# Performance work log

Measured on AMD Instinct MI355X. Metric: run time of the kernel, lower is better.

## Reference

```python
import jax, jax.numpy as jnp
import numpy as np

N = 50000   # nodes
E = 600000  # edges
D = 128     # in_channels == heads*hidden_channels
OUT = 64    # out_channels
L = 3       # local_layers
EPS = 1e-5  # BatchNorm eps


def setup_inputs() -> dict:
    key = jax.random.key(0)
    ks = jax.random.split(key, 10)
    s = 0.05
    x = jax.random.normal(ks[0], (N, D), jnp.float32)
    edge_index = jax.random.randint(ks[1], (2, E), 0, N, dtype=jnp.int32)
    Wg = jax.random.normal(ks[2], (L, D, D), jnp.float32) * s  # GCNConv weights
    bg = jnp.zeros((L, D), jnp.float32)                         # GCNConv biases
    Wl = jax.random.normal(ks[3], (L, D, D), jnp.float32) * s  # residual Linear weights
    bl = jax.random.normal(ks[4], (L, D), jnp.float32) * s
    gamma = jnp.ones((L, D), jnp.float32)                       # BN scale
    beta = jnp.zeros((L, D), jnp.float32)                       # BN shift
    Wp = jax.random.normal(ks[5], (D, OUT), jnp.float32) * s   # pred head
    bp = jnp.zeros((OUT,), jnp.float32)
    return {"x": x, "edge_index": edge_index, "Wg": Wg, "bg": bg,
            "Wl": Wl, "bl": bl, "gamma": gamma, "beta": beta,
            "Wp": Wp, "bp": bp}


def reference(x, edge_index, Wg, bg, Wl, bl, gamma, beta, Wp, bp):
    src, dst = edge_index[0], edge_index[1]
    # GCN symmetric normalization with self-loops (PyG gcn_norm):
    # deg computed on target (col) including self-loop.
    deg = jax.ops.segment_sum(jnp.ones((E,), x.dtype), dst, num_segments=N) + 1.0
    dinv = jax.lax.rsqrt(deg)                      # deg^{-1/2}, [N]
    enorm = dinv[src] * dinv[dst]                  # per-edge norm, [E]
    self_norm = (dinv * dinv)[:, None]             # deg^{-1} for self-loop, [N,1]

    h = x
    x_local = jnp.zeros((N, D), x.dtype)
    for i in range(L):
        hg = h @ Wg[i]                             # [N, D] transformed features
        # gather -> weight -> scatter-add (message passing) + self-loop term
        agg = jax.ops.segment_sum(hg[src] * enorm[:, None], dst, num_segments=N)
        conv = agg + hg * self_norm + bg[i]
        # residual linear
        h = conv + h @ Wl[i] + bl[i]
        # BatchNorm1d (training-mode batch statistics, biased var)
        mu = jnp.mean(h, axis=0)
        var = jnp.mean(jnp.square(h - mu), axis=0)
        h = (h - mu) * jax.lax.rsqrt(var + EPS) * gamma[i] + beta[i]
        h = jax.nn.relu(h)
        x_local = x_local + h                      # add_ accumulation
    return x_local @ Wp + bp
```

## Files before the change

kernel.cpp:

```cpp
#include <hip/hip_runtime.h>

#define D 128
#define OUTC 64
#define EC 256

typedef float floatx4 __attribute__((ext_vector_type(4)));
typedef short short8 __attribute__((ext_vector_type(8)));

__device__ inline unsigned short f2bf(float f) {
  unsigned int u = __float_as_uint(f);
  unsigned int r = (u + 0x7FFF + ((u >> 16) & 1)) >> 16;
  return (unsigned short)r;
}
__device__ inline float bf2f(unsigned short u) {
  return __uint_as_float(((unsigned int)u) << 16);
}

__device__ inline int swz(int row, int k) { return row * 128 + (k ^ ((row & 7) << 3)); }

__global__ __launch_bounds__(256) void k_prepx(const float* __restrict__ x, unsigned short* __restrict__ xb, int total4) {
  int stride = gridDim.x * blockDim.x;
  for (int i = blockIdx.x * blockDim.x + threadIdx.x; i < total4; i += stride) {
    float4 v = ((const float4*)x)[i];
    ushort4 o;
    o.x = f2bf(v.x); o.y = f2bf(v.y); o.z = f2bf(v.z); o.w = f2bf(v.w);
    ((ushort4*)xb)[i] = o;
  }
}

__global__ __launch_bounds__(256) void k_prepw(const float* __restrict__ Wg, const float* __restrict__ Wl,
                                               const float* __restrict__ Wp,
                                               unsigned short* __restrict__ Wgt, unsigned short* __restrict__ Wlt,
                                               unsigned short* __restrict__ Wpt) {
  int u = blockIdx.x * 256 + threadIdx.x;
  const int W1 = 3 * D * D;
  if (u < W1) {
    int i = u / (D * D), rem = u % (D * D);
    int k = rem / D, n = rem % D;
    Wgt[i * D * D + n * D + k] = f2bf(Wg[u]);
  } else if (u < 2 * W1) {
    int v = u - W1;
    int i = v / (D * D), rem = v % (D * D);
    int k = rem / D, n = rem % D;
    Wlt[i * D * D + n * D + k] = f2bf(Wl[v]);
  } else if (u < 2 * W1 + D * OUTC) {
    int v = u - 2 * W1;
    int k = v / OUTC, n = v % OUTC;
    Wpt[n * D + k] = f2bf(Wp[v]);
  }
}


__global__ __launch_bounds__(256) void k_bh(const int* __restrict__ dst, int* __restrict__ bh,
                                            int E, int nbuk, int chk) {
  __shared__ int hist[256];
  int t = threadIdx.x, c = blockIdx.x;
  hist[t] = 0;
  __syncthreads();
  int s = c * chk, e = min(E, s + chk);
  for (int j = s + t; j < e; j += 256)
    atomicAdd(&hist[dst[j] >> 8], 1);
  __syncthreads();
  if (t < nbuk) bh[t * EC + c] = hist[t];
}

__device__ inline int block_scan4(int4 v, int t, int* total) {
  int s = v.x + v.y + v.z + v.w;
  int lane = t & 63, w = t >> 6;
  int incl = s;
  #pragma unroll
  for (int off = 1; off < 64; off <<= 1) {
    int nb = __shfl_up(incl, off);
    if (lane >= off) incl += nb;
  }
  __shared__ int wsum[4];
  if (lane == 63) wsum[w] = incl;
  __syncthreads();
  int woff = 0;
  #pragma unroll
  for (int k = 0; k < 3; ++k) if (w > k) woff += wsum[k];
  if (total) *total = wsum[0] + wsum[1] + wsum[2] + wsum[3];
  return woff + incl - s;
}

__global__ __launch_bounds__(256) void k_gscan1(int* __restrict__ arr, int* __restrict__ bsum, int n) {
  int t = threadIdx.x;
  int i0 = blockIdx.x * 1024 + t * 4;
  int4 v = make_int4(0, 0, 0, 0);
  if (i0 + 3 < n) v = *(const int4*)(arr + i0);
  else {
    if (i0 < n) v.x = arr[i0];
    if (i0 + 1 < n) v.y = arr[i0 + 1];
    if (i0 + 2 < n) v.z = arr[i0 + 2];
    if (i0 + 3 < n) v.w = arr[i0 + 3];
  }
  int total;
  int e = block_scan4(v, t, &total);
  if (i0 < n) {
    int4 o;
    o.x = e; o.y = e + v.x; o.z = o.y + v.y; o.w = o.z + v.z;
    if (i0 + 3 < n) *(int4*)(arr + i0) = o;
    else {
      arr[i0] = o.x;
      if (i0 + 1 < n) arr[i0 + 1] = o.y;
      if (i0 + 2 < n) arr[i0 + 2] = o.z;
    }
  }
  if (t == 0) bsum[blockIdx.x] = total;
}

__global__ __launch_bounds__(256) void k_gscan2(int* __restrict__ bsum, int nb) {
  int t = threadIdx.x;
  int i0 = t * 4;
  int4 v = make_int4(0, 0, 0, 0);
  if (i0 + 3 < nb) v = *(const int4*)(bsum + i0);
  else {
    if (i0 < nb) v.x = bsum[i0];
    if (i0 + 1 < nb) v.y = bsum[i0 + 1];
    if (i0 + 2 < nb) v.z = bsum[i0 + 2];
    if (i0 + 3 < nb) v.w = bsum[i0 + 3];
  }
  int e = block_scan4(v, t, nullptr);
  if (i0 < nb) {
    bsum[i0] = e;
    if (i0 + 1 < nb) bsum[i0 + 1] = e + v.x;
    if (i0 + 2 < nb) bsum[i0 + 2] = e + v.x + v.y;
    if (i0 + 3 < nb) bsum[i0 + 3] = e + v.x + v.y + v.z;
  }
}

__global__ __launch_bounds__(256) void k_scatter(const int* __restrict__ src, const int* __restrict__ dst,
                                                 const int* __restrict__ bhs, const int* __restrict__ bsum,
                                                 unsigned int* __restrict__ ebuk, int E, int nbuk, int chk) {
  __shared__ int cur[256];
  int t = threadIdx.x, c = blockIdx.x;
  if (t < nbuk) {
    int idx = t * EC + c;
    cur[t] = bhs[idx] + bsum[idx >> 10];
  }
  __syncthreads();
  int s = c * chk, e = min(E, s + chk);
  for (int j = s + t; j < e; j += 256) {
    int d = dst[j];
    int pos = atomicAdd(&cur[d >> 8], 1);
    ebuk[pos] = (unsigned int)src[j] | ((unsigned int)(d & 255) << 24);
  }
}

__global__ __launch_bounds__(256) void k_csr(const unsigned int* __restrict__ ebuk, const int* __restrict__ bhs,
                                             const int* __restrict__ bsum,
                                             int* __restrict__ rowstart, int* __restrict__ csr,
                                             float* __restrict__ dinv, int E, int N, int nbuk) {
  __shared__ int cnt[256];
  __shared__ int wsum[4];
  int t = threadIdx.x, b = blockIdx.x;
  int si = b * EC;
  int s = bhs[si] + bsum[si >> 10];
  int e;
  if (b + 1 < nbuk) { int ei_ = (b + 1) * EC; e = bhs[ei_] + bsum[ei_ >> 10]; }
  else e = E;
  cnt[t] = 0;
  __syncthreads();
  for (int j = s + t; j < e; j += 256)
    atomicAdd(&cnt[ebuk[j] >> 24], 1);
  __syncthreads();
  int v = cnt[t];
  int lane = t & 63, w = t >> 6;
  int incl = v;
  #pragma unroll
  for (int off = 1; off < 64; off <<= 1) {
    int nb = __shfl_up(incl, off);
    if (lane >= off) incl += nb;
  }
  if (lane == 63) wsum[w] = incl;
  __syncthreads();
  int woff = 0;
  #pragma unroll
  for (int k = 0; k < 3; ++k) if (w > k) woff += wsum[k];
  int rs = s + woff + incl - v;
  int node = (b << 8) + t;
  __syncthreads();
  cnt[t] = rs;
  if (node < N) {
    rowstart[node] = rs;
    dinv[node] = rsqrtf((float)v + 1.0f);
  }
  if (node == 0) rowstart[N] = E;
  __syncthreads();
  for (int j = s + t; j < e; j += 256) {
    unsigned int ed = ebuk[j];
    int pos = atomicAdd(&cnt[ed >> 24], 1);
    csr[pos] = (int)(ed & 0xFFFFFFu);
  }
}

__global__ __launch_bounds__(256) void k_dual(const unsigned short* __restrict__ Ab,
                                              const unsigned short* __restrict__ Wgt,
                                              const unsigned short* __restrict__ Wlt,
                                              const float* __restrict__ bg, const float* __restrict__ bl,
                                              unsigned short* __restrict__ hg, unsigned short* __restrict__ hl, int M) {
  __shared__ unsigned short As[64 * 128];
  __shared__ unsigned short Bs[128 * 128];
  int tid = threadIdx.x;
  int row0 = blockIdx.x * 64;

  {
    int r = tid >> 2;
    int row = row0 + r;
    const unsigned short* src = Ab + (size_t)row * D;
    #pragma unroll
    for (int j = 0; j < 4; ++j) {
      int c = (tid & 3) + j * 4;
      short8 v = {0, 0, 0, 0, 0, 0, 0, 0};
      if (row < M) v = *(const short8*)(src + c * 8);
      *(short8*)&As[swz(r, c * 8)] = v;
    }
  }
  #pragma unroll
  for (int j = 0; j < 8; ++j) {
    int idx = tid + j * 256;
    int nr = idx >> 4, c = idx & 15;
    *(short8*)&Bs[swz(nr, c * 8)] = *(const short8*)(Wgt + nr * D + c * 8);
  }
  __syncthreads();

  int lane = tid & 63, w = tid >> 6;
  int lrow = lane & 15, lk = (lane >> 4) * 8;

  short8 af[4][4];
  #pragma unroll
  for (int m = 0; m < 4; ++m) {
    int ar = lrow + m * 16;
    #pragma unroll
    for (int kk = 0; kk < 4; ++kk)
      af[m][kk] = *(const short8*)&As[swz(ar, lk + kk * 32)];
  }

  {
    short8 bfg[2][4];
    #pragma unroll
    for (int n = 0; n < 2; ++n) {
      int br = w * 32 + n * 16 + lrow;
      #pragma unroll
      for (int kk = 0; kk < 4; ++kk)
        bfg[n][kk] = *(const short8*)&Bs[swz(br, lk + kk * 32)];
    }
    floatx4 acc[4][2];
    #pragma unroll
    for (int m = 0; m < 4; ++m)
      #pragma unroll
      for (int n = 0; n < 2; ++n)
        acc[m][n] = (floatx4)0.0f;
    #pragma unroll
    for (int kk = 0; kk < 4; ++kk)
      #pragma unroll
      for (int m = 0; m < 4; ++m)
        #pragma unroll
        for (int n = 0; n < 2; ++n)
          acc[m][n] = __builtin_amdgcn_mfma_f32_16x16x32_bf16(af[m][kk], bfg[n][kk], acc[m][n], 0, 0, 0);
    #pragma unroll
    for (int m = 0; m < 4; ++m)
      #pragma unroll
      for (int n = 0; n < 2; ++n) {
        int col = w * 32 + n * 16 + lrow;
        #pragma unroll
        for (int reg = 0; reg < 4; ++reg) {
          int row = row0 + m * 16 + (lane >> 4) * 4 + reg;
          if (row < M) hg[(size_t)row * D + col] = f2bf(acc[m][n][reg]);
        }
      }
  }
  __syncthreads();
  #pragma unroll
  for (int j = 0; j < 8; ++j) {
    int idx = tid + j * 256;
    int nr = idx >> 4, c = idx & 15;
    *(short8*)&Bs[swz(nr, c * 8)] = *(const short8*)(Wlt + nr * D + c * 8);
  }
  __syncthreads();
  {
    short8 bfl[2][4];
    #pragma unroll
    for (int n = 0; n < 2; ++n) {
      int br = w * 32 + n * 16 + lrow;
      #pragma unroll
      for (int kk = 0; kk < 4; ++kk)
        bfl[n][kk] = *(const short8*)&Bs[swz(br, lk + kk * 32)];
    }
    floatx4 acc[4][2];
    #pragma unroll
    for (int m = 0; m < 4; ++m)
      #pragma unroll
      for (int n = 0; n < 2; ++n)
        acc[m][n] = (floatx4)0.0f;
    #pragma unroll
    for (int kk = 0; kk < 4; ++kk)
      #pragma unroll
      for (int m = 0; m < 4; ++m)
        #pragma unroll
        for (int n = 0; n < 2; ++n)
          acc[m][n] = __builtin_amdgcn_mfma_f32_16x16x32_bf16(af[m][kk], bfl[n][kk], acc[m][n], 0, 0, 0);
    #pragma unroll
    for (int m = 0; m < 4; ++m)
      #pragma unroll
      for (int n = 0; n < 2; ++n) {
        int col = w * 32 + n * 16 + lrow;
        float bias = bg[col] + bl[col];
        #pragma unroll
        for (int reg = 0; reg < 4; ++reg) {
          int row = row0 + m * 16 + (lane >> 4) * 4 + reg;
          if (row < M) hl[(size_t)row * D + col] = f2bf(acc[m][n][reg] + bias);
        }
      }
  }
}

__global__ __launch_bounds__(256) void k_agg(const unsigned short* __restrict__ hg, unsigned short* __restrict__ pre,
                                             const int* __restrict__ rowstart, const int* __restrict__ csr,
                                             const float* __restrict__ dinv,
                                             float* __restrict__ partial, int n, int ABS) {
  int t = threadIdx.x, b = blockIdx.x;
  int w = t >> 6, lane = t & 63;
  const unsigned int* base = (const unsigned int*)hg;
  unsigned int* prew = (unsigned int*)pre;
  float st_s0 = 0.f, st_s1 = 0.f, st_q0 = 0.f, st_q1 = 0.f;
  int c = lane * 2;
  int node0 = b * 8 + w * 2;
  #pragma unroll 1
  for (int k = 0; k < 2; ++k) {
    int node = node0 + k;
    if (node >= n) break;
    int s = rowstart[node], e = rowstart[node + 1];
    float dn = dinv[node];
    unsigned int ps = base[(size_t)node * 64 + lane];
    unsigned int oldw = prew[(size_t)node * 64 + lane];
    float a0 = 0.f, a1 = 0.f, b0 = 0.f, b1 = 0.f;
    float c0 = 0.f, c1 = 0.f, d0 = 0.f, d1 = 0.f;
    int j = s;
    for (; j + 4 <= e; j += 4) {
      int sn0 = csr[j], sn1 = csr[j + 1], sn2 = csr[j + 2], sn3 = csr[j + 3];
      float w0 = dinv[sn0], w1 = dinv[sn1], w2 = dinv[sn2], w3 = dinv[sn3];
      unsigned int p0 = base[(size_t)sn0 * 64 + lane];
      unsigned int p1 = base[(size_t)sn1 * 64 + lane];
      unsigned int p2 = base[(size_t)sn2 * 64 + lane];
      unsigned int p3 = base[(size_t)sn3 * 64 + lane];
      a0 += w0 * __uint_as_float(p0 << 16); a1 += w0 * __uint_as_float(p0 & 0xFFFF0000u);
      b0 += w1 * __uint_as_float(p1 << 16); b1 += w1 * __uint_as_float(p1 & 0xFFFF0000u);
      c0 += w2 * __uint_as_float(p2 << 16); c1 += w2 * __uint_as_float(p2 & 0xFFFF0000u);
      d0 += w3 * __uint_as_float(p3 << 16); d1 += w3 * __uint_as_float(p3 & 0xFFFF0000u);
    }
    for (; j < e; ++j) {
      int sn = csr[j];
      float wv = dinv[sn];
      unsigned int p = base[(size_t)sn * 64 + lane];
      a0 += wv * __uint_as_float(p << 16);
      a1 += wv * __uint_as_float(p & 0xFFFF0000u);
    }
    float acc0 = (a0 + b0) + (c0 + d0);
    float acc1 = (a1 + b1) + (c1 + d1);
    float sf = dn * dn;
    float h0 = __uint_as_float(ps << 16);
    float h1 = __uint_as_float(ps & 0xFFFF0000u);
    float old0 = __uint_as_float(oldw << 16);
    float old1 = __uint_as_float(oldw & 0xFFFF0000u);
    float p0 = dn * acc0 + h0 * sf + old0;
    float p1 = dn * acc1 + h1 * sf + old1;
    prew[(size_t)node * 64 + lane] = (unsigned int)f2bf(p0) | ((unsigned int)f2bf(p1) << 16);
    st_s0 += p0; st_s1 += p1;
    st_q0 += p0 * p0; st_q1 += p1 * p1;
  }
  __shared__ float sm[4][128], sq[4][128];
  sm[w][c] = st_s0; sm[w][c + 1] = st_s1;
  sq[w][c] = st_q0; sq[w][c + 1] = st_q1;
  __syncthreads();
  if (t < 128) {
    float s = (sm[0][t] + sm[1][t]) + (sm[2][t] + sm[3][t]);
    float q = (sq[0][t] + sq[1][t]) + (sq[2][t] + sq[3][t]);
    partial[(size_t)t * ABS + b] = s;
    partial[(size_t)(128 + t) * ABS + b] = q;
  }
}

__global__ __launch_bounds__(256) void k_fin2(const float* __restrict__ partial,
                                              const float* __restrict__ gamma, const float* __restrict__ beta,
                                              float* __restrict__ ab, int nab, int ABS, float invN) {
  int cch = blockIdx.x;
  int t = threadIdx.x;
  const float* ps = partial + (size_t)cch * ABS;
  const float* pq = partial + (size_t)(128 + cch) * ABS;
  float s = 0.f, q = 0.f;
  for (int i = t; i < nab; i += 256) { s += ps[i]; q += pq[i]; }
  __shared__ float rs[256], rq[256];
  rs[t] = s; rq[t] = q;
  __syncthreads();
  if (t < 64) {
    s = (rs[t] + rs[t + 64]) + (rs[t + 128] + rs[t + 192]);
    q = (rq[t] + rq[t + 64]) + (rq[t + 128] + rq[t + 192]);
    #pragma unroll
    for (int off = 32; off; off >>= 1) {
      s += __shfl_down(s, off);
      q += __shfl_down(q, off);
    }
    if (t == 0) {
      float mean = s * invN;
      float var = q * invN - mean * mean;
      float inv = rsqrtf(var + 1e-5f);
      float g = gamma[cch];
      ab[cch] = g * inv;
      ab[128 + cch] = beta[cch] - mean * inv * g;
    }
  }
}

template<bool FIRST>
__global__ __launch_bounds__(256) void k_fused(const unsigned short* __restrict__ pre, const float* __restrict__ ab,
                                               const unsigned short* __restrict__ Wpt, const float* __restrict__ bp,
                                               const unsigned short* __restrict__ Wgt,
                                               const unsigned short* __restrict__ Wlt,
                                               const float* __restrict__ bgn, const float* __restrict__ bln,
                                               float* __restrict__ out, unsigned short* __restrict__ hg,
                                               unsigned short* __restrict__ hl, int M) {
  __shared__ unsigned short As[64 * 128];
  __shared__ unsigned short Bs[128 * 128];
  int tid = threadIdx.x;
  int row0 = blockIdx.x * 64;

  {
    int r = tid >> 2, qq = tid & 3;
    int row = row0 + r;
    bool valid = row < M;
    const unsigned short* Pp = pre + (size_t)row * D;
    #pragma unroll
    for (int ch = 0; ch < 4; ++ch) {
      int k0 = qq * 32 + ch * 8;
      short8 pv = {0, 0, 0, 0, 0, 0, 0, 0};
      if (valid) pv = *(const short8*)(Pp + k0);
      float4 a0 = *(const float4*)(ab + k0),        a1 = *(const float4*)(ab + k0 + 4);
      float4 b0 = *(const float4*)(ab + 128 + k0),  b1 = *(const float4*)(ab + 128 + k0 + 4);
      float av[8] = {a0.x, a0.y, a0.z, a0.w, a1.x, a1.y, a1.z, a1.w};
      float bv[8] = {b0.x, b0.y, b0.z, b0.w, b1.x, b1.y, b1.z, b1.w};
      unsigned short hv[8];
      #pragma unroll
      for (int jj = 0; jj < 8; ++jj) {
        float f = bf2f((unsigned short)pv[jj]);
        hv[jj] = f2bf(fmaxf(f * av[jj] + bv[jj], 0.f));
      }
      *(short8*)&As[swz(r, k0)] = *(const short8*)hv;
    }
  }
  #pragma unroll
  for (int j = 0; j < 4; ++j) {
    int idx = tid + j * 256;
    int nr = idx >> 4, c = idx & 15;
    *(short8*)&Bs[swz(nr, c * 8)] = *(const short8*)(Wpt + nr * D + c * 8);
  }
  __syncthreads();

  int lane = tid & 63, w = tid >> 6;
  int lrow = lane & 15, lk = (lane >> 4) * 8;

  short8 af[4][4];
  #pragma unroll
  for (int m = 0; m < 4; ++m) {
    int ar = lrow + m * 16;
    #pragma unroll
    for (int kk = 0; kk < 4; ++kk)
      af[m][kk] = *(const short8*)&As[swz(ar, lk + kk * 32)];
  }

  {
    short8 bfr[4];
    int br = w * 16 + lrow;
    #pragma unroll
    for (int kk = 0; kk < 4; ++kk)
      bfr[kk] = *(const short8*)&Bs[swz(br, lk + kk * 32)];
    floatx4 acc[4];
    #pragma unroll
    for (int m = 0; m < 4; ++m) acc[m] = (floatx4)0.0f;
    #pragma unroll
    for (int kk = 0; kk < 4; ++kk)
      #pragma unroll
      for (int m = 0; m < 4; ++m)
        acc[m] = __builtin_amdgcn_mfma_f32_16x16x32_bf16(af[m][kk], bfr[kk], acc[m], 0, 0, 0);
    int col = w * 16 + lrow;
    float bpv = FIRST ? bp[col] : 0.f;
    #pragma unroll
    for (int m = 0; m < 4; ++m)
      #pragma unroll
      for (int reg = 0; reg < 4; ++reg) {
        int row = row0 + m * 16 + (lane >> 4) * 4 + reg;
        if (row < M) {
          float* op = &out[(size_t)row * OUTC + col];
          float v = acc[m][reg] + bpv;
          if (!FIRST) v += *op;
          *op = v;
        }
      }
  }
  __syncthreads();
  #pragma unroll
  for (int j = 0; j < 8; ++j) {
    int idx = tid + j * 256;
    int nr = idx >> 4, c = idx & 15;
    *(short8*)&Bs[swz(nr, c * 8)] = *(const short8*)(Wgt + nr * D + c * 8);
  }
  __syncthreads();
  {
    short8 bfg[2][4];
    #pragma unroll
    for (int n = 0; n < 2; ++n) {
      int br = w * 32 + n * 16 + lrow;
      #pragma unroll
      for (int kk = 0; kk < 4; ++kk)
        bfg[n][kk] = *(const short8*)&Bs[swz(br, lk + kk * 32)];
    }
    floatx4 acc[4][2];
    #pragma unroll
    for (int m = 0; m < 4; ++m)
      #pragma unroll
      for (int n = 0; n < 2; ++n)
        acc[m][n] = (floatx4)0.0f;
    #pragma unroll
    for (int kk = 0; kk < 4; ++kk)
      #pragma unroll
      for (int m = 0; m < 4; ++m)
        #pragma unroll
        for (int n = 0; n < 2; ++n)
          acc[m][n] = __builtin_amdgcn_mfma_f32_16x16x32_bf16(af[m][kk], bfg[n][kk], acc[m][n], 0, 0, 0);
    #pragma unroll
    for (int m = 0; m < 4; ++m)
      #pragma unroll
      for (int n = 0; n < 2; ++n) {
        int col = w * 32 + n * 16 + lrow;
        #pragma unroll
        for (int reg = 0; reg < 4; ++reg) {
          int row = row0 + m * 16 + (lane >> 4) * 4 + reg;
          if (row < M) hg[(size_t)row * D + col] = f2bf(acc[m][n][reg]);
        }
      }
  }
  __syncthreads();
  #pragma unroll
  for (int j = 0; j < 8; ++j) {
    int idx = tid + j * 256;
    int nr = idx >> 4, c = idx & 15;
    *(short8*)&Bs[swz(nr, c * 8)] = *(const short8*)(Wlt + nr * D + c * 8);
  }
  __syncthreads();
  {
    short8 bfl[2][4];
    #pragma unroll
    for (int n = 0; n < 2; ++n) {
      int br = w * 32 + n * 16 + lrow;
      #pragma unroll
      for (int kk = 0; kk < 4; ++kk)
        bfl[n][kk] = *(const short8*)&Bs[swz(br, lk + kk * 32)];
    }
    floatx4 acc[4][2];
    #pragma unroll
    for (int m = 0; m < 4; ++m)
      #pragma unroll
      for (int n = 0; n < 2; ++n)
        acc[m][n] = (floatx4)0.0f;
    #pragma unroll
    for (int kk = 0; kk < 4; ++kk)
      #pragma unroll
      for (int m = 0; m < 4; ++m)
        #pragma unroll
        for (int n = 0; n < 2; ++n)
          acc[m][n] = __builtin_amdgcn_mfma_f32_16x16x32_bf16(af[m][kk], bfl[n][kk], acc[m][n], 0, 0, 0);
    #pragma unroll
    for (int m = 0; m < 4; ++m)
      #pragma unroll
      for (int n = 0; n < 2; ++n) {
        int col = w * 32 + n * 16 + lrow;
        float bias = bgn[col] + bln[col];
        #pragma unroll
        for (int reg = 0; reg < 4; ++reg) {
          int row = row0 + m * 16 + (lane >> 4) * 4 + reg;
          if (row < M) hl[(size_t)row * D + col] = f2bf(acc[m][n][reg] + bias);
        }
      }
  }
}

__global__ __launch_bounds__(256) void k_out(const unsigned short* __restrict__ pre, const float* __restrict__ ab,
                                             const unsigned short* __restrict__ Wpt,
                                             float* __restrict__ out, int M) {
  __shared__ unsigned short As[64 * 128];
  __shared__ unsigned short Bs[OUTC * 128];
  int tid = threadIdx.x;
  int row0 = blockIdx.x * 64;

  {
    int r = tid >> 2, qq = tid & 3;
    int row = row0 + r;
    bool valid = row < M;
    const unsigned short* Pp = pre + (size_t)row * D;
    #pragma unroll
    for (int ch = 0; ch < 4; ++ch) {
      int k0 = qq * 32 + ch * 8;
      short8 pv = {0, 0, 0, 0, 0, 0, 0, 0};
      if (valid) pv = *(const short8*)(Pp + k0);
      float4 a0 = *(const float4*)(ab + k0),        a1 = *(const float4*)(ab + k0 + 4);
      float4 b0 = *(const float4*)(ab + 128 + k0),  b1 = *(const float4*)(ab + 128 + k0 + 4);
      float av[8] = {a0.x, a0.y, a0.z, a0.w, a1.x, a1.y, a1.z, a1.w};
      float bv[8] = {b0.x, b0.y, b0.z, b0.w, b1.x, b1.y, b1.z, b1.w};
      unsigned short hv[8];
      #pragma unroll
      for (int jj = 0; jj < 8; ++jj) {
        float f = bf2f((unsigned short)pv[jj]);
        hv[jj] = f2bf(fmaxf(f * av[jj] + bv[jj], 0.f));
      }
      *(short8*)&As[swz(r, k0)] = *(const short8*)hv;
    }
  }
  #pragma unroll
  for (int j = 0; j < 4; ++j) {
    int idx = tid + j * 256;
    int nr = idx >> 4, c = idx & 15;
    *(short8*)&Bs[swz(nr, c * 8)] = *(const short8*)(Wpt + nr * D + c * 8);
  }
  __syncthreads();

  int lane = tid & 63, w = tid >> 6;
  int lrow = lane & 15, lk = (lane >> 4) * 8;

  short8 af[4][4];
  #pragma unroll
  for (int m = 0; m < 4; ++m) {
    int ar = lrow + m * 16;
    #pragma unroll
    for (int kk = 0; kk < 4; ++kk)
      af[m][kk] = *(const short8*)&As[swz(ar, lk + kk * 32)];
  }
  short8 bfr[4];
  {
    int br = w * 16 + lrow;
    #pragma unroll
    for (int kk = 0; kk < 4; ++kk)
      bfr[kk] = *(const short8*)&Bs[swz(br, lk + kk * 32)];
  }
  floatx4 acc[4];
  #pragma unroll
  for (int m = 0; m < 4; ++m) acc[m] = (floatx4)0.0f;
  #pragma unroll
  for (int kk = 0; kk < 4; ++kk)
    #pragma unroll
    for (int m = 0; m < 4; ++m)
      acc[m] = __builtin_amdgcn_mfma_f32_16x16x32_bf16(af[m][kk], bfr[kk], acc[m], 0, 0, 0);

  int col = w * 16 + lrow;
  #pragma unroll
  for (int m = 0; m < 4; ++m)
    #pragma unroll
    for (int reg = 0; reg < 4; ++reg) {
      int row = row0 + m * 16 + (lane >> 4) * 4 + reg;
      if (row < M) {
        float* op = &out[(size_t)row * OUTC + col];
        *op = *op + acc[m][reg];
      }
    }
}

extern "C" void kernel_launch(void* const* d_in, const int* in_sizes, int n_in,
                              void* d_out, int out_size, void* d_ws, size_t ws_size,
                              hipStream_t stream) {
  const float* x     = (const float*)d_in[0];
  const int*   ei    = (const int*)d_in[1];
  const float* Wg    = (const float*)d_in[2];
  const float* bg    = (const float*)d_in[3];
  const float* Wl    = (const float*)d_in[4];
  const float* bl    = (const float*)d_in[5];
  const float* gamma = (const float*)d_in[6];
  const float* beta  = (const float*)d_in[7];
  const float* Wp    = (const float*)d_in[8];
  const float* bp    = (const float*)d_in[9];
  float* out = (float*)d_out;

  int N = in_sizes[0] / D;
  int E = in_sizes[1] / 2;
  const int* srcp = ei;
  const int* dstp = ei + E;

  char* wsb = (char*)d_ws;
  size_t off = 0;
  auto alloc = [&](size_t bytes) {
    off = (off + 255) & ~(size_t)255;
    void* p = wsb + off;
    off += bytes;
    return p;
  };
  int nab = (N + 7) / 8;
  int ABS = (nab + 63) & ~63;
  float* dinv     = (float*)alloc((size_t)N * 4);
  int*   rowstart = (int*)alloc((size_t)(N + 1) * 4);
  int*   csr      = (int*)alloc((size_t)E * 4);
  int*   bh       = (int*)alloc((size_t)256 * EC * 4);
  unsigned int* ebuk = (unsigned int*)alloc((size_t)E * 4);
  int*   bsum     = (int*)alloc(1024 * 4);
  float* partial  = (float*)alloc((size_t)256 * ABS * 4);
  float* ab       = (float*)alloc(3 * 256 * 4);
  unsigned short* xb  = (unsigned short*)alloc((size_t)N * D * 2);
  unsigned short* hg  = (unsigned short*)alloc((size_t)N * D * 2);
  unsigned short* hl  = (unsigned short*)alloc((size_t)N * D * 2);
  unsigned short* Wgt = (unsigned short*)alloc(3 * D * D * 2);
  unsigned short* Wlt = (unsigned short*)alloc(3 * D * D * 2);
  unsigned short* Wpt = (unsigned short*)alloc(D * OUTC * 2);
  (void)ws_size; (void)n_in; (void)out_size;

  k_prepx<<<1024, 256, 0, stream>>>(x, xb, N * D / 4);
  int wtotal = 2 * 3 * D * D + D * OUTC;
  k_prepw<<<(wtotal + 255) / 256, 256, 0, stream>>>(Wg, Wl, Wp, Wgt, Wlt, Wpt);

  int nbuk = (N + 255) >> 8;
  int chk  = (E + EC - 1) / EC;
  k_bh<<<EC, 256, 0, stream>>>(dstp, bh, E, nbuk, chk);
  int sn  = nbuk * EC;
  int snb = (sn + 1023) >> 10;
  k_gscan1<<<snb, 256, 0, stream>>>(bh, bsum, sn);
  k_gscan2<<<1, 256, 0, stream>>>(bsum, snb);
  k_scatter<<<EC, 256, 0, stream>>>(srcp, dstp, bh, bsum, ebuk, E, nbuk, chk);
  k_csr<<<nbuk, 256, 0, stream>>>(ebuk, bh, bsum, rowstart, csr, dinv, E, N, nbuk);

  int mt = (N + 63) / 64;
  float invN = 1.0f / (float)N;

  k_dual<<<mt, 256, 0, stream>>>(xb, Wgt, Wlt, bg, bl, hg, hl, N);

  for (int i = 0; i < 3; ++i) {
    k_agg<<<nab, 256, 0, stream>>>(hg, hl, rowstart, csr, dinv, partial, N, ABS);
    k_fin2<<<128, 256, 0, stream>>>(partial, gamma + (size_t)i * D, beta + (size_t)i * D,
                                    ab + i * 256, nab, ABS, invN);
    if (i == 0)
      k_fused<true><<<mt, 256, 0, stream>>>(hl, ab + i * 256, Wpt, bp,
                                            Wgt + (size_t)(i + 1) * D * D, Wlt + (size_t)(i + 1) * D * D,
                                            bg + (size_t)(i + 1) * D, bl + (size_t)(i + 1) * D,
                                            out, hg, hl, N);
    else if (i == 1)
      k_fused<false><<<mt, 256, 0, stream>>>(hl, ab + i * 256, Wpt, bp,
                                             Wgt + (size_t)(i + 1) * D * D, Wlt + (size_t)(i + 1) * D * D,
                                             bg + (size_t)(i + 1) * D, bl + (size_t)(i + 1) * D,
                                             out, hg, hl, N);
    else
      k_out<<<mt, 256, 0, stream>>>(hl, ab + i * 256, Wpt, out, N);
  }
}
```

Baseline: 299.7 us.

## Process four nodes per wave in aggregation and split BN stat reduction into two stages

Each aggregation wave now handles four destination nodes instead of two, which halves the block count and the number of per-block partial statistic rows. The partial sums are stored row-major per block. They are reduced by a 64-block coalesced pass followed by a single-block finalize, replacing the per-channel strided reduction kernel. This trades some aggregation parallelism for a cheaper, more coalesced batch-norm statistics reduction, at the cost of one extra small kernel launch per layer.

Result: faster. 290.3 us (-3.1%).

```diff
diff --git a/kernel.cpp b/kernel.cpp
--- a/kernel.cpp
+++ b/kernel.cpp
@@ -318,16 +318,16 @@
 __global__ __launch_bounds__(256) void k_agg(const unsigned short* __restrict__ hg, unsigned short* __restrict__ pre,
                                              const int* __restrict__ rowstart, const int* __restrict__ csr,
                                              const float* __restrict__ dinv,
-                                             float* __restrict__ partial, int n, int ABS) {
+                                             float* __restrict__ partial, int n) {
   int t = threadIdx.x, b = blockIdx.x;
   int w = t >> 6, lane = t & 63;
   const unsigned int* base = (const unsigned int*)hg;
   unsigned int* prew = (unsigned int*)pre;
   float st_s0 = 0.f, st_s1 = 0.f, st_q0 = 0.f, st_q1 = 0.f;
   int c = lane * 2;
-  int node0 = b * 8 + w * 2;
+  int node0 = b * 16 + w * 4;
   #pragma unroll 1
-  for (int k = 0; k < 2; ++k) {
+  for (int k = 0; k < 4; ++k) {
     int node = node0 + k;
     if (node >= n) break;
     int s = rowstart[node], e = rowstart[node + 1];
@@ -376,39 +376,37 @@
   if (t < 128) {
     float s = (sm[0][t] + sm[1][t]) + (sm[2][t] + sm[3][t]);
     float q = (sq[0][t] + sq[1][t]) + (sq[2][t] + sq[3][t]);
-    partial[(size_t)t * ABS + b] = s;
-    partial[(size_t)(128 + t) * ABS + b] = q;
-  }
-}
-
-__global__ __launch_bounds__(256) void k_fin2(const float* __restrict__ partial,
+    partial[(size_t)b * 256 + t] = s;
+    partial[(size_t)b * 256 + 128 + t] = q;
+  }
+}
+
+__global__ __launch_bounds__(256) void k_fina(const float* __restrict__ partial, float* __restrict__ p2, int nab) {
+  int t = threadIdx.x, b = blockIdx.x;
+  float s = 0.f;
+  for (int i = b; i < nab; i += 64)
+    s += partial[(size_t)i * 256 + t];
+  p2[(size_t)b * 256 + t] = s;
+}
+
+__global__ __launch_bounds__(256) void k_finb(const float* __restrict__ p2,
                                               const float* __restrict__ gamma, const float* __restrict__ beta,
-                                              float* __restrict__ ab, int nab, int ABS, float invN) {
-  int cch = blockIdx.x;
+                                              float* __restrict__ ab, float invN) {
   int t = threadIdx.x;
-  const float* ps = partial + (size_t)cch * ABS;
-  const float* pq = partial + (size_t)(128 + cch) * ABS;
-  float s = 0.f, q = 0.f;
-  for (int i = t; i < nab; i += 256) { s += ps[i]; q += pq[i]; }
-  __shared__ float rs[256], rq[256];
-  rs[t] = s; rq[t] = q;
-  __syncthreads();
-  if (t < 64) {
-    s = (rs[t] + rs[t + 64]) + (rs[t + 128] + rs[t + 192]);
-    q = (rq[t] + rq[t + 64]) + (rq[t + 128] + rq[t + 192]);
-    #pragma unroll
-    for (int off = 32; off; off >>= 1) {
-      s += __shfl_down(s, off);
-      q += __shfl_down(q, off);
-    }
-    if (t == 0) {
-      float mean = s * invN;
-      float var = q * invN - mean * mean;
-      float inv = rsqrtf(var + 1e-5f);
-      float g = gamma[cch];
-      ab[cch] = g * inv;
-      ab[128 + cch] = beta[cch] - mean * inv * g;
-    }
+  float s = 0.f;
+  #pragma unroll
+  for (int b = 0; b < 64; ++b)
+    s += p2[(size_t)b * 256 + t];
+  __shared__ float red[256];
+  red[t] = s;
+  __syncthreads();
+  if (t < 128) {
+    float mean = red[t] * invN;
+    float var = red[128 + t] * invN - mean * mean;
+    float inv = rsqrtf(var + 1e-5f);
+    float g = gamma[t];
+    ab[t] = g * inv;
+    ab[128 + t] = beta[t] - mean * inv * g;
   }
 }
 
@@ -691,15 +689,15 @@
     off += bytes;
     return p;
   };
-  int nab = (N + 7) / 8;
-  int ABS = (nab + 63) & ~63;
+  int nab = (N + 15) / 16;
   float* dinv     = (float*)alloc((size_t)N * 4);
   int*   rowstart = (int*)alloc((size_t)(N + 1) * 4);
   int*   csr      = (int*)alloc((size_t)E * 4);
   int*   bh       = (int*)alloc((size_t)256 * EC * 4);
   unsigned int* ebuk = (unsigned int*)alloc((size_t)E * 4);
   int*   bsum     = (int*)alloc(1024 * 4);
-  float* partial  = (float*)alloc((size_t)256 * ABS * 4);
+  float* partial  = (float*)alloc((size_t)nab * 256 * 4);
+  float* p2       = (float*)alloc((size_t)64 * 256 * 4);
   float* ab       = (float*)alloc(3 * 256 * 4);
   unsigned short* xb  = (unsigned short*)alloc((size_t)N * D * 2);
   unsigned short* hg  = (unsigned short*)alloc((size_t)N * D * 2);
@@ -729,9 +727,9 @@
   k_dual<<<mt, 256, 0, stream>>>(xb, Wgt, Wlt, bg, bl, hg, hl, N);
 
   for (int i = 0; i < 3; ++i) {
-    k_agg<<<nab, 256, 0, stream>>>(hg, hl, rowstart, csr, dinv, partial, N, ABS);
-    k_fin2<<<128, 256, 0, stream>>>(partial, gamma + (size_t)i * D, beta + (size_t)i * D,
-                                    ab + i * 256, nab, ABS, invN);
+    k_agg<<<nab, 256, 0, stream>>>(hg, hl, rowstart, csr, dinv, partial, N);
+    k_fina<<<64, 256, 0, stream>>>(partial, p2, nab);
+    k_finb<<<1, 256, 0, stream>>>(p2, gamma + (size_t)i * D, beta + (size_t)i * D, ab + i * 256, invN);
     if (i == 0)
       k_fused<true><<<mt, 256, 0, stream>>>(hl, ab + i * 256, Wpt, bp,
                                             Wgt + (size_t)(i + 1) * D * D, Wlt + (size_t)(i + 1) * D * D,
```
